# Kernel optimization log

Hardware: AMD Instinct MI355X
Metric: run time of the kernel (lower is better)

## Reference

```python
import jax, jax.numpy as jnp
import numpy as np

B = 16384   # number of subgraphs per view
S = 4       # subgraph size (CoLA fixed)
N = B * S   # nodes per batched graph
D = 300     # in_feats
O = 64      # out_feats
TAU = 0.5
BETA = 0.0  # generative_loss_w
EPS = 1e-05


def _make_edges():
    # fully connected (incl. self loops) within each 4-node subgraph
    base = np.arange(B, dtype=np.int64) * S
    a = np.arange(S, dtype=np.int64)
    src = (base[:, None, None] + a[None, :, None] + 0 * a[None, None, :]).reshape(-1)
    dst = (base[:, None, None] + 0 * a[None, :, None] + a[None, None, :]).reshape(-1)
    return jnp.asarray(src), jnp.asarray(dst)


def setup_inputs() -> dict:
    key = jax.random.key(0)
    ks = jax.random.split(key, 14)
    src, dst = _make_edges()
    E = src.shape[0]
    sc = 0.05
    inp = {
        'pos_feat': jax.random.normal(ks[0], (N, D), jnp.float32),
        'pos_src': src, 'pos_dst': dst,
        'pos_w': jax.random.uniform(ks[1], (E,), jnp.float32),
        'neg_feat': jax.random.normal(ks[2], (N, D), jnp.float32),
        'neg_src': src, 'neg_dst': dst,
        'neg_w': jax.random.uniform(ks[3], (E,), jnp.float32),
        'aug_feat': jax.random.normal(ks[4], (N, D), jnp.float32),
        'aug_src': src, 'aug_dst': dst,
        'aug_w': jax.random.uniform(ks[5], (E,), jnp.float32),
        'W': jax.random.normal(ks[6], (D, O), jnp.float32) * sc,
        'bias': jnp.zeros((O,), jnp.float32),
        'prelu_a': jnp.asarray(0.25, jnp.float32),
        'Ws': jax.random.normal(ks[7], (O, O), jnp.float32) * sc,
        'bs': jnp.zeros((O,), jnp.float32),
        'Wg': jax.random.normal(ks[8], (O, O), jnp.float32) * sc,
        'bg': jnp.zeros((O,), jnp.float32),
        'Wa1': jax.random.normal(ks[9], (O, O), jnp.float32) * sc,
        'ba1': jnp.zeros((O,), jnp.float32),
        'Wa2': jax.random.normal(ks[10], (O, D), jnp.float32) * sc,
        'ba2': jnp.zeros((D,), jnp.float32),
    }
    return inp


def _prelu(x, a):
    return jnp.where(x >= 0, x, a * x)


def _l2norm(x):
    n = jnp.sqrt(jnp.sum(x * x, axis=1, keepdims=True))
    return x / jnp.maximum(n, 1e-12)


def _gcn_branch(feat, src, dst, ew, W, bias, a, Ws, bs, Wg, bg):
    # OneLayerGCNWithGlobalAdg: zero anchor rows, pre-linear, weighted sum aggregation
    anchor = feat[::4]                       # [B, D]
    featz = feat.at[::4].set(0.0)
    anchor_out = _prelu(anchor @ W + bias, a)
    x = featz @ W                            # [N, O]
    msg = ew[:, None] * x[src]               # gather + scale
    h = jax.ops.segment_sum(msg, dst, num_segments=feat.shape[0])  # scatter-add
    h = _prelu(h + bias, a)
    pool = h.reshape(-1, 4, h.shape[1]).mean(axis=1)  # AvgPooling per subgraph
    pool_emb = _l2norm(pool @ Ws + bs)
    gcn_emb = _l2norm(h[::4] @ Wg + bg)
    return pool_emb, _l2norm(anchor_out), gcn_emb


def reference(pos_feat, pos_src, pos_dst, pos_w,
              neg_feat, neg_src, neg_dst, neg_w,
              aug_feat, aug_src, aug_dst, aug_w,
              W, bias, prelu_a, Ws, bs, Wg, bg, Wa1, ba1, Wa2, ba2):
    # eval mode: dropout is identity (and its output is unused in the original anyway,
    # since the gcn re-reads bg.ndata['feat'])
    anchor_inputs = pos_feat[::4]            # node 0 of each subgraph, pre-zeroing
    p_pool, p_anchor, p_gcn = _gcn_branch(pos_feat, pos_src, pos_dst, pos_w, W, bias, prelu_a, Ws, bs, Wg, bg)
    n_pool, n_anchor, n_gcn = _gcn_branch(neg_feat, neg_src, neg_dst, neg_w, W, bias, prelu_a, Ws, bs, Wg, bg)
    _ = _gcn_branch(aug_feat, aug_src, aug_dst, aug_w, W, bias, prelu_a, Ws, bs, Wg, bg)  # computed but unused (faithful)

    # InfoNCE over pooled embeddings
    pos_score_pool = jnp.exp(jnp.sum(p_pool * p_anchor, axis=1) / TAU)          # [B]
    neg_all = jnp.exp((p_anchor @ n_pool.T) / TAU).sum(axis=1)                  # [B] (dense BxB exp)
    neg_score_pool = neg_all / neg_all.shape[0]
    loss_pool = -jnp.log(pos_score_pool / (neg_all + EPS))

    # generative loss (attr_mlp on pos gcn emb)
    pred = jax.nn.relu(jax.nn.relu(p_gcn @ Wa1 + ba1) @ Wa2 + ba2)
    _ = jax.nn.relu(jax.nn.relu(n_gcn @ Wa1 + ba1) @ Wa2 + ba2)  # neg pred unused (faithful)
    loss_gen = jnp.linalg.norm(anchor_inputs - pred) / anchor_inputs.shape[1]
    pos_score_gen = -loss_gen

    loss = loss_pool + loss_gen * BETA
    pos_score = pos_score_pool + pos_score_gen * BETA
    neg_score = neg_score_pool + 0.0 * BETA
    return (loss, pos_score, neg_score)
```

## Files before the change

### kernel.cpp

```cpp
#include <hip/hip_runtime.h>
#include <stdint.h>

#define NGRP 16384
#define DIM  300
#define ODIM 64
#define KPAD 320
#define JC   32

#define EXP2SCALE 2.8853900817779268f

typedef __attribute__((ext_vector_type(8))) short bf16x8;
typedef __attribute__((ext_vector_type(4))) float f32x4;

static __device__ __forceinline__ unsigned short f2bf(float f) {
  union { float f; unsigned u; } x; x.f = f;
  unsigned r = x.u + 0x7fffu + ((x.u >> 16) & 1u);
  return (unsigned short)(r >> 16);
}

static __device__ __forceinline__ bf16x8 pack8(float4 a, float4 b) {
  union { bf16x8 v; uint32_t u[4]; } r;
  asm("v_cvt_pk_bf16_f32 %0, %1, %2" : "=v"(r.u[0]) : "v"(a.x), "v"(a.y));
  asm("v_cvt_pk_bf16_f32 %0, %1, %2" : "=v"(r.u[1]) : "v"(a.z), "v"(a.w));
  asm("v_cvt_pk_bf16_f32 %0, %1, %2" : "=v"(r.u[2]) : "v"(b.x), "v"(b.y));
  asm("v_cvt_pk_bf16_f32 %0, %1, %2" : "=v"(r.u[3]) : "v"(b.z), "v"(b.w));
  return r.v;
}

static __device__ __forceinline__ float red32(float v) {
  v += __shfl_xor(v, 1); v += __shfl_xor(v, 2); v += __shfl_xor(v, 4);
  v += __shfl_xor(v, 8); v += __shfl_xor(v, 16);
  return v;
}

__global__ __launch_bounds__(256) void prep_wt(const float* __restrict__ W,
                                               unsigned short* __restrict__ wt) {
  int o = blockIdx.x * 256 + threadIdx.x;
  if (o >= ODIM * KPAD) return;
  int n = o / KPAD, k = o % KPAD;
  float v = (k < DIM) ? W[(size_t)k * ODIM + n] : 0.f;
  wt[o] = f2bf(v);
}

template <bool POS>
__global__ __launch_bounds__(256) void branch_mfma(
    const float* __restrict__ feat, const float* __restrict__ ew,
    const unsigned short* __restrict__ wt, const float* __restrict__ bias,
    const float* __restrict__ prelu_a, const float* __restrict__ Ws,
    const float* __restrict__ bs,
    unsigned short* __restrict__ emb,
    float* __restrict__ pos_dot)
{
  __shared__ float lds_pool[32][65];
  __shared__ float lds_anchor[32][65];
  const int tid = threadIdx.x, wid = tid >> 6, lane = tid & 63;
  const int lm = lane & 15, lh = lane >> 4;
  const int wrow = blockIdx.x * 128 + wid * 32;

  const float* ap[2];
  const unsigned short* bp[4];
  #pragma unroll
  for (int rt = 0; rt < 2; ++rt)
    ap[rt] = feat + (size_t)(wrow + rt * 16 + lm) * DIM + lh * 8;
  #pragma unroll
  for (int ct = 0; ct < 4; ++ct)
    bp[ct] = wt + (size_t)(ct * 16 + lm) * KPAD + lh * 8;

  f32x4 acc[2][4];
  #pragma unroll
  for (int rt = 0; rt < 2; ++rt)
    #pragma unroll
    for (int ct = 0; ct < 4; ++ct) acc[rt][ct] = (f32x4){0.f, 0.f, 0.f, 0.f};

  #pragma unroll
  for (int step = 0; step < 9; ++step) {
    const int k0 = step * 32;
    bf16x8 a[2], b[4];
    #pragma unroll
    for (int ct = 0; ct < 4; ++ct) b[ct] = *(const bf16x8*)(bp[ct] + k0);
    #pragma unroll
    for (int rt = 0; rt < 2; ++rt) {
      const float* p = ap[rt] + k0;
      a[rt] = pack8(*(const float4*)p, *(const float4*)(p + 4));
    }
    #pragma unroll
    for (int rt = 0; rt < 2; ++rt)
      #pragma unroll
      for (int ct = 0; ct < 4; ++ct)
        acc[rt][ct] = __builtin_amdgcn_mfma_f32_16x16x32_bf16(a[rt], b[ct], acc[rt][ct], 0, 0, 0);
  }
  {
    bf16x8 a[2], b[4];
    #pragma unroll
    for (int ct = 0; ct < 4; ++ct) b[ct] = *(const bf16x8*)(bp[ct] + 288);
    #pragma unroll
    for (int rt = 0; rt < 2; ++rt) {
      float4 f0 = {0.f, 0.f, 0.f, 0.f}, f1 = {0.f, 0.f, 0.f, 0.f};
      const float* p = ap[rt] + 288;
      if (lh == 0) { f0 = *(const float4*)p; f1 = *(const float4*)(p + 4); }
      else if (lh == 1) { f0 = *(const float4*)p; }
      a[rt] = pack8(f0, f1);
    }
    #pragma unroll
    for (int rt = 0; rt < 2; ++rt)
      #pragma unroll
      for (int ct = 0; ct < 4; ++ct)
        acc[rt][ct] = __builtin_amdgcn_mfma_f32_16x16x32_bf16(a[rt], b[ct], acc[rt][ct], 0, 0, 0);
  }

  const float pa = prelu_a[0];
  float bc[4];
  #pragma unroll
  for (int ct = 0; ct < 4; ++ct) bc[ct] = bias[ct * 16 + lm];

  #pragma unroll
  for (int rt = 0; rt < 2; ++rt) {
    const int gblk = wid * 8 + rt * 4 + lh;
    const size_t grp = (size_t)blockIdx.x * 32 + gblk;
    const float* e = ew + grp * 16;
    float w1[4], w2[4], w3[4];
    #pragma unroll
    for (int j = 0; j < 4; ++j) { w1[j] = e[4 + j]; w2[j] = e[8 + j]; w3[j] = e[12 + j]; }
    #pragma unroll
    for (int ct = 0; ct < 4; ++ct) {
      const int c = ct * 16 + lm;
      const float x0 = acc[rt][ct][0], x1 = acc[rt][ct][1];
      const float x2 = acc[rt][ct][2], x3 = acc[rt][ct][3];
      float pool = 0.f;
      #pragma unroll
      for (int j = 0; j < 4; ++j) {
        float h = fmaf(w1[j], x1, fmaf(w2[j], x2, w3[j] * x3)) + bc[ct];
        h = (h >= 0.f) ? h : pa * h;
        pool += h;
      }
      lds_pool[gblk][c] = pool * 0.25f;
      if (POS) {
        float av = x0 + bc[ct];
        av = (av >= 0.f) ? av : pa * av;
        lds_anchor[gblk][c] = av;
      }
    }
  }
  __syncthreads();

  const int c2 = (tid & 31) * 2;
  const int g0 = (tid >> 5) * 4;
  float y[4][2];
  { const float b0 = bs[c2], b1 = bs[c2 + 1];
    #pragma unroll
    for (int j = 0; j < 4; ++j) { y[j][0] = b0; y[j][1] = b1; } }
  for (int o = 0; o < ODIM; o += 4) {
    float4 pv[4];
    #pragma unroll
    for (int j = 0; j < 4; ++j) pv[j] = *(const float4*)&lds_pool[g0 + j][o];
    #pragma unroll
    for (int u = 0; u < 4; ++u) {
      float2 w = *(const float2*)(Ws + (size_t)(o + u) * ODIM + c2);
      #pragma unroll
      for (int j = 0; j < 4; ++j) {
        const float p = (&pv[j].x)[u];
        y[j][0] = fmaf(p, w.x, y[j][0]);
        y[j][1] = fmaf(p, w.y, y[j][1]);
      }
    }
  }
  #pragma unroll
  for (int j = 0; j < 4; ++j) {
    const size_t grp = (size_t)blockIdx.x * 32 + g0 + j;
    float s = red32(y[j][0] * y[j][0] + y[j][1] * y[j][1]);
    const float inv = 1.f / fmaxf(sqrtf(s), 1e-12f);
    if (POS) {
      const float a0 = lds_anchor[g0 + j][c2], a1 = lds_anchor[g0 + j][c2 + 1];
      float s2 = red32(a0 * a0 + a1 * a1);
      const float inv2 = 1.f / fmaxf(sqrtf(s2), 1e-12f);
      float dot = red32(a0 * y[j][0] + a1 * y[j][1]) * inv * inv2;
      if ((tid & 31) == 0) pos_dot[grp] = dot;
      const float sc = inv2 * EXP2SCALE;
      ushort2 st; st.x = f2bf(a0 * sc); st.y = f2bf(a1 * sc);
      *(ushort2*)(emb + grp * ODIM + c2) = st;
    } else {
      ushort2 st; st.x = f2bf(y[j][0] * inv); st.y = f2bf(y[j][1] * inv);
      *(ushort2*)(emb + grp * ODIM + c2) = st;
    }
  }
}

__global__ __launch_bounds__(256) void score_kernel(
    const unsigned short* __restrict__ pa, const unsigned short* __restrict__ npl,
    float* __restrict__ partial)
{
  __shared__ unsigned short kv[4 * 16 * 72];
  const int tid = threadIdx.x;
  const int wid = tid >> 6, lane = tid & 63;
  const int lm = lane & 15, lh = lane >> 4;
  const int rwb = blockIdx.x * 256 + wid * 64;
  const int jbase = blockIdx.y * (NGRP / JC);

  bf16x8 af[4][2];
  #pragma unroll
  for (int mt = 0; mt < 4; ++mt) {
    const unsigned short* ap = pa + (size_t)(rwb + mt * 16 + lm) * ODIM + lh * 8;
    af[mt][0] = *(const bf16x8*)(ap);
    af[mt][1] = *(const bf16x8*)(ap + 32);
  }

  float s[4][4];
  #pragma unroll
  for (int mt = 0; mt < 4; ++mt)
    #pragma unroll
    for (int r = 0; r < 4; ++r) s[mt][r] = 0.f;

  const unsigned short* src = npl + (size_t)jbase * ODIM;
  const int g1 = tid + 256;
  const int d0 = (tid >> 7) * 1152 + ((tid >> 3) & 15) * 72 + (tid & 7) * 8;
  const int d1 = (g1  >> 7) * 1152 + ((g1  >> 3) & 15) * 72 + (g1  & 7) * 8;
  const int ro = lm * 72 + lh * 8;

  bf16x8 ld0 = *(const bf16x8*)(src + tid * 8);
  bf16x8 ld1 = *(const bf16x8*)(src + g1 * 8);

  for (int it = 0; it < 8; ++it) {
    *(bf16x8*)&kv[d0] = ld0;
    *(bf16x8*)&kv[d1] = ld1;
    __syncthreads();
    if (it < 7) {
      const unsigned short* ns = src + (it + 1) * 4096;
      ld0 = *(const bf16x8*)(ns + tid * 8);
      ld1 = *(const bf16x8*)(ns + g1 * 8);
    }
    #pragma unroll
    for (int tt = 0; tt < 4; ++tt) {
      const unsigned short* kp = &kv[tt * 1152 + ro];
      bf16x8 b0 = *(const bf16x8*)(kp);
      bf16x8 b1 = *(const bf16x8*)(kp + 32);
      #pragma unroll
      for (int mt = 0; mt < 4; ++mt) {
        f32x4 d = {0.f, 0.f, 0.f, 0.f};
        d = __builtin_amdgcn_mfma_f32_16x16x32_bf16(af[mt][0], b0, d, 0, 0, 0);
        d = __builtin_amdgcn_mfma_f32_16x16x32_bf16(af[mt][1], b1, d, 0, 0, 0);
        #pragma unroll
        for (int r = 0; r < 4; ++r) s[mt][r] += __builtin_amdgcn_exp2f(d[r]);
      }
    }
    __syncthreads();
  }

  #pragma unroll
  for (int mt = 0; mt < 4; ++mt)
    #pragma unroll
    for (int r = 0; r < 4; ++r) {
      float v = s[mt][r];
      v += __shfl_xor(v, 1); v += __shfl_xor(v, 2);
      v += __shfl_xor(v, 4); v += __shfl_xor(v, 8);
      s[mt][r] = v;
    }

  if (lm == 0) {
    float* pr = partial + (size_t)blockIdx.y * NGRP + rwb + lh * 4;
    #pragma unroll
    for (int mt = 0; mt < 4; ++mt)
      #pragma unroll
      for (int r = 0; r < 4; ++r)
        pr[mt * 16 + r] = s[mt][r];
  }
}

__global__ __launch_bounds__(256) void final_kernel(
    const float* __restrict__ pos_dot, const float* __restrict__ partial,
    float* __restrict__ out)
{
  const int i = blockIdx.x * 256 + threadIdx.x;
  float na = 0.f;
  #pragma unroll
  for (int c = 0; c < JC; ++c) na += partial[(size_t)c * NGRP + i];
  float ps = expf(pos_dot[i] * 2.0f);
  out[i]             = -logf(ps / (na + 1e-5f));
  out[NGRP + i]      = ps;
  out[2 * NGRP + i]  = na * (1.0f / (float)NGRP);
}

extern "C" void kernel_launch(void* const* d_in, const int* in_sizes, int n_in,
                              void* d_out, int out_size, void* d_ws, size_t ws_size,
                              hipStream_t stream) {
  const float* pos_feat = (const float*)d_in[0];
  const float* pos_w    = (const float*)d_in[3];
  const float* neg_feat = (const float*)d_in[4];
  const float* neg_w    = (const float*)d_in[7];
  const float* W        = (const float*)d_in[12];
  const float* bias     = (const float*)d_in[13];
  const float* prelu_a  = (const float*)d_in[14];
  const float* Ws       = (const float*)d_in[15];
  const float* bs       = (const float*)d_in[16];

  char* ws = (char*)d_ws;
  unsigned short* pa_bf   = (unsigned short*)(ws);
  unsigned short* np_bf   = (unsigned short*)(ws + (2u << 20));
  float*          partial = (float*)(ws + (4u << 20));
  float*          pos_dot = (float*)(ws + (6u << 20));
  unsigned short* wt      = (unsigned short*)(ws + (6u << 20) + (64u << 10));

  prep_wt<<<(ODIM * KPAD + 255) / 256, 256, 0, stream>>>(W, wt);
  branch_mfma<true ><<<NGRP / 32, 256, 0, stream>>>(pos_feat, pos_w, wt, bias,
                                                    prelu_a, Ws, bs, pa_bf, pos_dot);
  branch_mfma<false><<<NGRP / 32, 256, 0, stream>>>(neg_feat, neg_w, wt, bias,
                                                    prelu_a, Ws, bs, np_bf, nullptr);
  score_kernel<<<dim3(NGRP / 256, JC), 256, 0, stream>>>(pa_bf, np_bf, partial);
  final_kernel<<<NGRP / 256, 256, 0, stream>>>(pos_dot, partial, (float*)d_out);
}
```

Baseline: 116.5 us.

## Stage GCN weight in LDS and double score-kernel chunk per sync

The branch kernel now copies the padded bf16 weight matrix into shared memory once per block, with a padded row stride, and reads the B fragments from LDS instead of global memory. The score kernel loads 128 negative rows per iteration instead of 64, halving the number of barrier-separated iterations. Both changes raise LDS use per block (about 42KB extra in the branch kernel), which may lower occupancy. The extra prologue copy and barrier also add latency before the MFMA loop starts.

```diff
diff --git a/kernel.cpp b/kernel.cpp
--- a/kernel.cpp
+++ b/kernel.cpp
@@ -5,6 +5,7 @@
 #define DIM  300
 #define ODIM 64
 #define KPAD 320
+#define WPAD 328
 #define JC   32
 
 #define EXP2SCALE 2.8853900817779268f
@@ -51,33 +52,43 @@
     unsigned short* __restrict__ emb,
     float* __restrict__ pos_dot)
 {
+  __shared__ unsigned short wlds[ODIM * WPAD];
   __shared__ float lds_pool[32][65];
   __shared__ float lds_anchor[32][65];
   const int tid = threadIdx.x, wid = tid >> 6, lane = tid & 63;
   const int lm = lane & 15, lh = lane >> 4;
   const int wrow = blockIdx.x * 128 + wid * 32;
 
+  #pragma unroll
+  for (int k = 0; k < 10; ++k) {
+    const int c = tid + k * 256;
+    const int row = c / 40, off = (c % 40) * 8;
+    *(bf16x8*)&wlds[row * WPAD + off] = *(const bf16x8*)(wt + row * KPAD + off);
+  }
+
   const float* ap[2];
-  const unsigned short* bp[4];
   #pragma unroll
   for (int rt = 0; rt < 2; ++rt)
     ap[rt] = feat + (size_t)(wrow + rt * 16 + lm) * DIM + lh * 8;
+  const unsigned short* bl[4];
   #pragma unroll
   for (int ct = 0; ct < 4; ++ct)
-    bp[ct] = wt + (size_t)(ct * 16 + lm) * KPAD + lh * 8;
+    bl[ct] = &wlds[(ct * 16 + lm) * WPAD + lh * 8];
 
   f32x4 acc[2][4];
   #pragma unroll
   for (int rt = 0; rt < 2; ++rt)
     #pragma unroll
     for (int ct = 0; ct < 4; ++ct) acc[rt][ct] = (f32x4){0.f, 0.f, 0.f, 0.f};
+
+  __syncthreads();
 
   #pragma unroll
   for (int step = 0; step < 9; ++step) {
     const int k0 = step * 32;
     bf16x8 a[2], b[4];
     #pragma unroll
-    for (int ct = 0; ct < 4; ++ct) b[ct] = *(const bf16x8*)(bp[ct] + k0);
+    for (int ct = 0; ct < 4; ++ct) b[ct] = *(const bf16x8*)(bl[ct] + k0);
     #pragma unroll
     for (int rt = 0; rt < 2; ++rt) {
       const float* p = ap[rt] + k0;
@@ -92,7 +103,7 @@
   {
     bf16x8 a[2], b[4];
     #pragma unroll
-    for (int ct = 0; ct < 4; ++ct) b[ct] = *(const bf16x8*)(bp[ct] + 288);
+    for (int ct = 0; ct < 4; ++ct) b[ct] = *(const bf16x8*)(bl[ct] + 288);
     #pragma unroll
     for (int rt = 0; rt < 2; ++rt) {
       float4 f0 = {0.f, 0.f, 0.f, 0.f}, f1 = {0.f, 0.f, 0.f, 0.f};
@@ -189,7 +200,7 @@
     const unsigned short* __restrict__ pa, const unsigned short* __restrict__ npl,
     float* __restrict__ partial)
 {
-  __shared__ unsigned short kv[4 * 16 * 72];
+  __shared__ unsigned short kv[8 * 16 * 72];
   const int tid = threadIdx.x;
   const int wid = tid >> 6, lane = tid & 63;
   const int lm = lane & 15, lh = lane >> 4;
@@ -211,25 +222,34 @@
     for (int r = 0; r < 4; ++r) s[mt][r] = 0.f;
 
   const unsigned short* src = npl + (size_t)jbase * ODIM;
-  const int g1 = tid + 256;
-  const int d0 = (tid >> 7) * 1152 + ((tid >> 3) & 15) * 72 + (tid & 7) * 8;
-  const int d1 = (g1  >> 7) * 1152 + ((g1  >> 3) & 15) * 72 + (g1  & 7) * 8;
+  int dd[4];
+  #pragma unroll
+  for (int k = 0; k < 4; ++k) {
+    const int g = tid + k * 256;
+    dd[k] = (g >> 7) * 1152 + ((g >> 3) & 15) * 72 + (g & 7) * 8;
+  }
   const int ro = lm * 72 + lh * 8;
 
-  bf16x8 ld0 = *(const bf16x8*)(src + tid * 8);
-  bf16x8 ld1 = *(const bf16x8*)(src + g1 * 8);
-
-  for (int it = 0; it < 8; ++it) {
-    *(bf16x8*)&kv[d0] = ld0;
-    *(bf16x8*)&kv[d1] = ld1;
+  bf16x8 ld0 = *(const bf16x8*)(src + (tid          ) * 8);
+  bf16x8 ld1 = *(const bf16x8*)(src + (tid + 256    ) * 8);
+  bf16x8 ld2 = *(const bf16x8*)(src + (tid + 512    ) * 8);
+  bf16x8 ld3 = *(const bf16x8*)(src + (tid + 768    ) * 8);
+
+  for (int it = 0; it < 4; ++it) {
+    *(bf16x8*)&kv[dd[0]] = ld0;
+    *(bf16x8*)&kv[dd[1]] = ld1;
+    *(bf16x8*)&kv[dd[2]] = ld2;
+    *(bf16x8*)&kv[dd[3]] = ld3;
     __syncthreads();
-    if (it < 7) {
-      const unsigned short* ns = src + (it + 1) * 4096;
-      ld0 = *(const bf16x8*)(ns + tid * 8);
-      ld1 = *(const bf16x8*)(ns + g1 * 8);
-    }
-    #pragma unroll
-    for (int tt = 0; tt < 4; ++tt) {
+    if (it < 3) {
+      const unsigned short* ns = src + (it + 1) * 8192;
+      ld0 = *(const bf16x8*)(ns + (tid      ) * 8);
+      ld1 = *(const bf16x8*)(ns + (tid + 256) * 8);
+      ld2 = *(const bf16x8*)(ns + (tid + 512) * 8);
+      ld3 = *(const bf16x8*)(ns + (tid + 768) * 8);
+    }
+    #pragma unroll
+    for (int tt = 0; tt < 8; ++tt) {
       const unsigned short* kp = &kv[tt * 1152 + ro];
       bf16x8 b0 = *(const bf16x8*)(kp);
       bf16x8 b1 = *(const bf16x8*)(kp + 32);
```

Result: slower. 136.1 us (+16.9%).
